# Performance work log

Measured on AMD Instinct MI355X. Metric: run time of the kernel, lower is better.

Reference implementation:

```python
import jax, jax.numpy as jnp
import numpy as np

NUM_USERS = 100000
NUM_ITEMS = 50000
N = NUM_USERS + NUM_ITEMS
EMB = 64
NNZ = 4000000
B = 4096
GAMMA = 1.0
REG_LAMBDA = 1e-4
T_END = 1.0  # Euler step size: t = [0, 1]
EPS = 1e-12


def setup_inputs() -> dict:
    key = jax.random.key(0)
    ks = jax.random.split(key, 8)
    user = jax.random.randint(ks[0], (B,), 0, NUM_USERS)
    positive = jax.random.randint(ks[1], (B,), 0, NUM_ITEMS)
    negative = jax.random.randint(ks[2], (B,), 0, NUM_ITEMS)
    adj_rows = jax.random.randint(ks[3], (NNZ,), 0, N)
    adj_cols = jax.random.randint(ks[4], (NNZ,), 0, N)
    # normalized-adjacency-like small positive values
    adj_vals = jax.random.uniform(ks[5], (NNZ,), jnp.float32) * 1e-3
    user_emb = jax.random.normal(ks[6], (NUM_USERS, EMB), jnp.float32) * 0.1
    item_emb = jax.random.normal(ks[7], (NUM_ITEMS, EMB), jnp.float32) * 0.1
    return {
        "user": user, "positive": positive, "negative": negative,
        "adj_rows": adj_rows, "adj_cols": adj_cols, "adj_vals": adj_vals,
        "user_emb": user_emb, "item_emb": item_emb,
    }


def _normalize(x):
    return x * jax.lax.rsqrt(jnp.sum(x * x, axis=-1, keepdims=True) + EPS)


def _uniform_loss(x):
    # log mean_{i<j} exp(-2 * ||xn_i - xn_j||^2), xn = L2-normalized
    xn = _normalize(x)
    sq = jnp.maximum(2.0 - 2.0 * (xn @ xn.T), 0.0)  # [B, B] pairwise squared dist
    mask = jnp.triu(jnp.ones((x.shape[0], x.shape[0]), bool), k=1)
    vals = jnp.where(mask, jnp.exp(-2.0 * sq), 0.0)
    n_pairs = x.shape[0] * (x.shape[0] - 1) / 2.0
    return jnp.log(jnp.sum(vals) / n_pairs)


def reference(user, positive, negative, adj_rows, adj_cols, adj_vals, user_emb, item_emb):
    # ego embeddings: concat user/item tables -> [N, EMB]
    x = jnp.concatenate([user_emb, item_emb], axis=0)
    # sparse spmm: ax = A @ x (COO gather + segment reduce)
    ax = jax.ops.segment_sum(adj_vals[:, None] * x[adj_cols], adj_rows, num_segments=N)
    # ODEFunc f(t, x) = A@x + e with e = x0; one Euler step z1 = x0 + t*(A@x0 + x0)
    z = x + T_END * (ax + x)
    u_all, i_all = z[:NUM_USERS], z[NUM_USERS:]
    u = u_all[user]          # [B, EMB]
    i = i_all[positive]      # [B, EMB]
    # alignment loss on normalized embeddings
    un, inn = _normalize(u), _normalize(i)
    align = jnp.mean(jnp.sum((un - inn) ** 2, axis=-1))
    # uniformity loss
    uniform = GAMMA * (_uniform_loss(u) + _uniform_loss(i)) / 2.0
    # L2 reg on ego (pre-propagation) embeddings
    ego_u = user_emb[user]
    ego_i = item_emb[positive]
    reg = REG_LAMBDA * 0.5 * (jnp.sum(ego_u ** 2) + jnp.sum(ego_i ** 2)) / B
    return jnp.stack([align, uniform, reg])
```

## Files before the change

kernel.cpp:

```cpp
#include <hip/hip_runtime.h>
#include <math.h>

#define NUSERS 100000
#define NITEMS 50000
#define NN (NUSERS + NITEMS)
#define EMB 64
#define NNZ_ 4000000
#define BB 4096
#define NSLOT (2 * BB)
#define CAP 128
#define FSTR 32
#define BMW 4688
#define EPSN 1e-12f
#define NT 32
#define NTRI 528


typedef __attribute__((ext_vector_type(8))) short short8v;
typedef __attribute__((ext_vector_type(16))) float f32x16;

__device__ inline float wave_reduce_sum(float v) {
  #pragma unroll
  for (int off = 32; off >= 1; off >>= 1) v += __shfl_xor(v, off, 64);
  return v;
}

__device__ inline unsigned short f2bf(float f) {
  unsigned u = __float_as_uint(f);
  unsigned r = u + 0x7fffu + ((u >> 16) & 1u);
  return (unsigned short)(r >> 16);
}

__global__ __launch_bounds__(256) void lg_init(int* map, int* fillp, unsigned* bitmap) {
  int t = blockIdx.x * blockDim.x + threadIdx.x;
  if (t < NN) map[t] = -1;
  if (t < NSLOT * FSTR) fillp[t] = 0;
  if (t < BMW) bitmap[t] = 0u;
}

__global__ __launch_bounds__(256) void lg_mark(const int* __restrict__ user,
                                               const int* __restrict__ positive,
                                               int* __restrict__ map,
                                               unsigned* __restrict__ bitmap) {
  int t = blockIdx.x * blockDim.x + threadIdx.x;
  if (t >= 2 * BB) return;
  int row = (t < BB) ? user[t] : (NUSERS + positive[t - BB]);
  atomicCAS(&map[row], -1, t);
  atomicOr(&bitmap[row >> 5], 1u << (row & 31));
}

__global__ __launch_bounds__(256) void lg_scan_bin(const int4* __restrict__ rows4,
                                                   const int4* __restrict__ cols4,
                                                   const float4* __restrict__ vals4,
                                                   const unsigned* __restrict__ bitmap,
                                                   const int* __restrict__ map,
                                                   int* __restrict__ fillp,
                                                   uint2* __restrict__ bins) {
  __shared__ int qr[4][256];
  __shared__ uint2 qcv[4][256];
  int t = threadIdx.x;
  int lane = t & 63, w = t >> 6;
  unsigned long long lmlt = (1ull << lane) - 1ull;
  const int NG = NNZ_ / 4;
  int g = blockIdx.x * 256 + t;
  bool valid = g < NG;
  int gg = valid ? g : 0;
  int4 r = rows4[gg];
  int4 c = cols4[gg];
  float4 v = vals4[gg];
  bool h0 = valid && ((bitmap[r.x >> 5] >> (r.x & 31)) & 1u);
  bool h1 = valid && ((bitmap[r.y >> 5] >> (r.y & 31)) & 1u);
  bool h2 = valid && ((bitmap[r.z >> 5] >> (r.z & 31)) & 1u);
  bool h3 = valid && ((bitmap[r.w >> 5] >> (r.w & 31)) & 1u);
  int qn = 0;
  {
    unsigned long long m = __ballot(h0);
    if (h0) { int p = qn + (int)__popcll(m & lmlt); qr[w][p] = r.x;
              qcv[w][p] = make_uint2((unsigned)c.x, __float_as_uint(v.x)); }
    qn += (int)__popcll(m);
  }
  {
    unsigned long long m = __ballot(h1);
    if (h1) { int p = qn + (int)__popcll(m & lmlt); qr[w][p] = r.y;
              qcv[w][p] = make_uint2((unsigned)c.y, __float_as_uint(v.y)); }
    qn += (int)__popcll(m);
  }
  {
    unsigned long long m = __ballot(h2);
    if (h2) { int p = qn + (int)__popcll(m & lmlt); qr[w][p] = r.z;
              qcv[w][p] = make_uint2((unsigned)c.z, __float_as_uint(v.z)); }
    qn += (int)__popcll(m);
  }
  {
    unsigned long long m = __ballot(h3);
    if (h3) { int p = qn + (int)__popcll(m & lmlt); qr[w][p] = r.w;
              qcv[w][p] = make_uint2((unsigned)c.w, __float_as_uint(v.w)); }
    qn += (int)__popcll(m);
  }
  for (int i = lane; i < qn; i += 64) {
    int rr = qr[w][i];
    uint2 cv = qcv[w][i];
    int s = map[rr];
    int pos = atomicAdd(&fillp[s * FSTR], 1);
    if (pos < CAP) bins[(size_t)s * CAP + pos] = cv;
  }
}

__global__ __launch_bounds__(256) void lg_accum(const int* __restrict__ fillp,
                                                const uint2* __restrict__ bins,
                                                const float* __restrict__ uemb,
                                                const float* __restrict__ iemb,
                                                float* __restrict__ acc) {
  int w = (blockIdx.x * blockDim.x + threadIdx.x) >> 6;
  int lane = threadIdx.x & 63;
  if (w >= NSLOT) return;
  int n = min(fillp[w * FSTR], CAP);
  const uint2* bs = bins + (size_t)w * CAP;
  float a = 0.0f;
  int k = 0;
  for (; k + 4 <= n; k += 4) {
    uint2 e0 = bs[k];
    uint2 e1 = bs[k + 1];
    uint2 e2 = bs[k + 2];
    uint2 e3 = bs[k + 3];
    int c0 = (int)e0.x; float v0 = __uint_as_float(e0.y);
    int c1 = (int)e1.x; float v1 = __uint_as_float(e1.y);
    int c2 = (int)e2.x; float v2 = __uint_as_float(e2.y);
    int c3 = (int)e3.x; float v3 = __uint_as_float(e3.y);
    const float* x0 = (c0 < NUSERS) ? uemb + (size_t)c0 * EMB : iemb + (size_t)(c0 - NUSERS) * EMB;
    const float* x1 = (c1 < NUSERS) ? uemb + (size_t)c1 * EMB : iemb + (size_t)(c1 - NUSERS) * EMB;
    const float* x2 = (c2 < NUSERS) ? uemb + (size_t)c2 * EMB : iemb + (size_t)(c2 - NUSERS) * EMB;
    const float* x3 = (c3 < NUSERS) ? uemb + (size_t)c3 * EMB : iemb + (size_t)(c3 - NUSERS) * EMB;
    float f0 = x0[lane], f1 = x1[lane], f2 = x2[lane], f3 = x3[lane];
    a = fmaf(v0, f0, a);
    a = fmaf(v1, f1, a);
    a = fmaf(v2, f2, a);
    a = fmaf(v3, f3, a);
  }
  for (; k < n; ++k) {
    uint2 e0 = bs[k];
    int c0 = (int)e0.x; float v0 = __uint_as_float(e0.y);
    const float* x0 = (c0 < NUSERS) ? uemb + (size_t)c0 * EMB : iemb + (size_t)(c0 - NUSERS) * EMB;
    a = fmaf(v0, x0[lane], a);
  }
  acc[(size_t)w * EMB + lane] = a;
}

__global__ __launch_bounds__(256) void lg_prep(const int* __restrict__ user,
                                               const int* __restrict__ positive,
                                               const float* __restrict__ uemb,
                                               const float* __restrict__ iemb,
                                               const int* __restrict__ map,
                                               const float* __restrict__ acc,
                                               unsigned short* __restrict__ zub,
                                               unsigned short* __restrict__ zib,
                                               float* __restrict__ part_align,
                                               float* __restrict__ part_reg) {
  int w = (blockIdx.x * blockDim.x + threadIdx.x) >> 6;
  int lane = threadIdx.x & 63;
  if (w >= BB) return;
  int ru = user[w];
  int pi = positive[w];
  float eu = uemb[(size_t)ru * EMB + lane];
  float ei = iemb[(size_t)pi * EMB + lane];
  int su = map[ru];
  int si = map[NUSERS + pi];
  float zul = 2.0f * eu + acc[(size_t)su * EMB + lane];
  float zil = 2.0f * ei + acc[(size_t)si * EMB + lane];
  float nu = wave_reduce_sum(zul * zul);
  float ni = wave_reduce_sum(zil * zil);
  float un = zul * rsqrtf(nu + EPSN);
  float inn = zil * rsqrtf(ni + EPSN);
  zub[(size_t)w * EMB + lane] = f2bf(un);
  zib[(size_t)w * EMB + lane] = f2bf(inn);
  float d = un - inn;
  float align_b = wave_reduce_sum(d * d);
  float reg_b = wave_reduce_sum(eu * eu + ei * ei);
  if (lane == 0) {
    part_align[w] = align_b;
    part_reg[w] = reg_b;
  }
}

__global__ __launch_bounds__(256) void lg_gram_mfma(const unsigned short* __restrict__ zub,
                                                    const unsigned short* __restrict__ zib,
                                                    float* __restrict__ gpart) {
  int L = blockIdx.x, m = blockIdx.y;
  int ib = 0, rem = L;
  while (rem >= NT - ib) { rem -= NT - ib; ++ib; }
  int jb = ib + rem;
  const unsigned short* z = (m == 0) ? zub : zib;
  __shared__ uint4 As4[1024];
  __shared__ uint4 Bs4[1024];
  __shared__ float wsum[4];
  int t = threadIdx.x;
  const uint4* srcA = (const uint4*)(z + (size_t)ib * 128 * EMB);
  const uint4* srcB = (const uint4*)(z + (size_t)jb * 128 * EMB);
  #pragma unroll
  for (int it = 0; it < 4; ++it) {
    int idx = it * 256 + t;
    int r = idx >> 3, s = idx & 7;
    int dst = r * 8 + (s ^ (r & 7));
    As4[dst] = srcA[idx];
    Bs4[dst] = srcB[idx];
  }
  __syncthreads();
  int l = t & 63, w = t >> 6;
  int wr = w >> 1, wc = w & 1;
  int lr = l & 31;
  int h = l >> 5;
  int ra0 = wr * 64 + lr;
  int ra1 = ra0 + 32;
  int rb0 = wc * 64 + lr;
  int rb1 = rb0 + 32;
  f32x16 a00 = {}, a01 = {}, a10 = {}, a11 = {};
  #pragma unroll
  for (int ks = 0; ks < 4; ++ks) {
    int seg = ks * 2 + h;
    short8v a0 = *(const short8v*)&As4[ra0 * 8 + (seg ^ (ra0 & 7))];
    short8v a1 = *(const short8v*)&As4[ra1 * 8 + (seg ^ (ra1 & 7))];
    short8v b0 = *(const short8v*)&Bs4[rb0 * 8 + (seg ^ (rb0 & 7))];
    short8v b1 = *(const short8v*)&Bs4[rb1 * 8 + (seg ^ (rb1 & 7))];
    a00 = __builtin_amdgcn_mfma_f32_32x32x16_bf16(a0, b0, a00, 0, 0, 0);
    a01 = __builtin_amdgcn_mfma_f32_32x32x16_bf16(a0, b1, a01, 0, 0, 0);
    a10 = __builtin_amdgcn_mfma_f32_32x32x16_bf16(a1, b0, a10, 0, 0, 0);
    a11 = __builtin_amdgcn_mfma_f32_32x32x16_bf16(a1, b1, a11, 0, 0, 0);
  }
  float s = 0.0f;
  #pragma unroll
  for (int e = 0; e < 16; ++e) {
    s += __expf(-2.0f * fmaxf(fmaf(-2.0f, a00[e], 2.0f), 0.0f));
    s += __expf(-2.0f * fmaxf(fmaf(-2.0f, a01[e], 2.0f), 0.0f));
    s += __expf(-2.0f * fmaxf(fmaf(-2.0f, a10[e], 2.0f), 0.0f));
    s += __expf(-2.0f * fmaxf(fmaf(-2.0f, a11[e], 2.0f), 0.0f));
  }
  s = wave_reduce_sum(s);
  if (l == 0) wsum[w] = s;
  __syncthreads();
  if (t == 0) {
    float tot = wsum[0] + wsum[1] + wsum[2] + wsum[3];
    float wgt = (ib == jb) ? 1.0f : 2.0f;
    gpart[m * NTRI + L] = wgt * tot;
  }
}

__global__ __launch_bounds__(256) void lg_final(const float* __restrict__ part_align,
                                                const float* __restrict__ part_reg,
                                                const float* __restrict__ gpart,
                                                float* __restrict__ out) {
  __shared__ float red[4][4];
  int t = threadIdx.x;
  float sa = 0.0f, sr = 0.0f, su = 0.0f, si = 0.0f;
  for (int k = t; k < 4096; k += 256) {
    sa += part_align[k];
    sr += part_reg[k];
  }
  for (int k = t; k < NTRI; k += 256) {
    su += gpart[k];
    si += gpart[NTRI + k];
  }
  sa = wave_reduce_sum(sa);
  sr = wave_reduce_sum(sr);
  su = wave_reduce_sum(su);
  si = wave_reduce_sum(si);
  if ((t & 63) == 0) {
    int wid = t >> 6;
    red[wid][0] = sa; red[wid][1] = sr; red[wid][2] = su; red[wid][3] = si;
  }
  __syncthreads();
  if (t == 0) {
    float a = 0, r = 0, Su = 0, Si = 0;
    #pragma unroll
    for (int wv = 0; wv < 4; ++wv) {
      a += red[wv][0]; r += red[wv][1]; Su += red[wv][2]; Si += red[wv][3];
    }
    float align = a / (float)BB;
    float reg = 1e-4f * 0.5f * r / (float)BB;
    float npairs = (float)BB * (float)(BB - 1) * 0.5f;
    float tri_u = (Su - (float)BB) * 0.5f;
    float tri_i = (Si - (float)BB) * 0.5f;
    float Lu = logf(tri_u / npairs);
    float Li = logf(tri_i / npairs);
    out[0] = align;
    out[1] = 0.5f * (Lu + Li);
    out[2] = reg;
  }
}

extern "C" void kernel_launch(void* const* d_in, const int* in_sizes, int n_in,
                              void* d_out, int out_size, void* d_ws, size_t ws_size,
                              hipStream_t stream) {
  const int* user = (const int*)d_in[0];
  const int* positive = (const int*)d_in[1];
  const int* adj_rows = (const int*)d_in[3];
  const int* adj_cols = (const int*)d_in[4];
  const float* adj_vals = (const float*)d_in[5];
  const float* uemb = (const float*)d_in[6];
  const float* iemb = (const float*)d_in[7];

  char* ws = (char*)d_ws;
  int* map = (int*)(ws);
  int* fillp = (int*)(ws + (1u << 20));
  uint2* bins = (uint2*)(ws + (2u << 20));
  float* acc = (float*)(ws + (10u << 20));
  unsigned short* zub = (unsigned short*)(ws + (12u << 20));
  unsigned short* zib = (unsigned short*)(ws + (12u << 20) + (512u << 10));
  float* part_align = (float*)(ws + (13u << 20));
  float* part_reg = (float*)(ws + (13u << 20) + (16u << 10));
  float* gpart = (float*)(ws + (13u << 20) + (32u << 10));
  unsigned* bitmap = (unsigned*)(ws + (13u << 20) + (64u << 10));
  float* out = (float*)d_out;

  const int NG = NNZ_ / 4;
  lg_init<<<dim3(1024), dim3(256), 0, stream>>>(map, fillp, bitmap);
  lg_mark<<<dim3(32), dim3(256), 0, stream>>>(user, positive, map, bitmap);
  lg_scan_bin<<<dim3((NG + 255) / 256), dim3(256), 0, stream>>>(
      (const int4*)adj_rows, (const int4*)adj_cols, (const float4*)adj_vals,
      bitmap, map, fillp, bins);
  lg_accum<<<dim3(NSLOT / 4), dim3(256), 0, stream>>>(fillp, bins, uemb, iemb, acc);
  lg_prep<<<dim3(1024), dim3(256), 0, stream>>>(user, positive, uemb, iemb, map,
                                                acc, zub, zib, part_align, part_reg);
  lg_gram_mfma<<<dim3(NTRI, 2), dim3(256), 0, stream>>>(zub, zib, gpart);
  lg_final<<<dim3(1), dim3(256), 0, stream>>>(part_align, part_reg, gpart, out);
}
```

Before: 62.41 us.

## Make scan-bin kernel persistent with grid-stride loop and prefetched next chunk

The COO scan/bin kernel now launches a fixed 1024-block grid, and each thread walks four strided chunks of the edge list. It prefetches the next int4/float4 rows, cols and vals while testing bitmap membership for the current chunk. The per-wave LDS queue grows to 512 entries and is flushed to the bins when nearly full, so fewer blocks are launched and load latency is hidden behind the bitmap checks. The cost is more shared memory per block, which may lower occupancy, plus the loop's serial dependency.

After: 64.83 us. 1.04x slower.

```diff
diff --git a/kernel.cpp b/kernel.cpp
--- a/kernel.cpp
+++ b/kernel.cpp
@@ -14,6 +14,8 @@
 #define EPSN 1e-12f
 #define NT 32
 #define NTRI 528
+#define SCAN_GRID 1024
+#define QCAP 512
 
 
 typedef __attribute__((ext_vector_type(8))) short short8v;
@@ -56,46 +58,66 @@
                                                    const int* __restrict__ map,
                                                    int* __restrict__ fillp,
                                                    uint2* __restrict__ bins) {
-  __shared__ int qr[4][256];
-  __shared__ uint2 qcv[4][256];
+  __shared__ int qr[4][QCAP];
+  __shared__ uint2 qcv[4][QCAP];
   int t = threadIdx.x;
   int lane = t & 63, w = t >> 6;
   unsigned long long lmlt = (1ull << lane) - 1ull;
   const int NG = NNZ_ / 4;
+  const int STR = SCAN_GRID * 256;
+  int qn = 0;
   int g = blockIdx.x * 256 + t;
-  bool valid = g < NG;
-  int gg = valid ? g : 0;
-  int4 r = rows4[gg];
-  int4 c = cols4[gg];
-  float4 v = vals4[gg];
-  bool h0 = valid && ((bitmap[r.x >> 5] >> (r.x & 31)) & 1u);
-  bool h1 = valid && ((bitmap[r.y >> 5] >> (r.y & 31)) & 1u);
-  bool h2 = valid && ((bitmap[r.z >> 5] >> (r.z & 31)) & 1u);
-  bool h3 = valid && ((bitmap[r.w >> 5] >> (r.w & 31)) & 1u);
-  int qn = 0;
-  {
-    unsigned long long m = __ballot(h0);
-    if (h0) { int p = qn + (int)__popcll(m & lmlt); qr[w][p] = r.x;
-              qcv[w][p] = make_uint2((unsigned)c.x, __float_as_uint(v.x)); }
-    qn += (int)__popcll(m);
-  }
-  {
-    unsigned long long m = __ballot(h1);
-    if (h1) { int p = qn + (int)__popcll(m & lmlt); qr[w][p] = r.y;
-              qcv[w][p] = make_uint2((unsigned)c.y, __float_as_uint(v.y)); }
-    qn += (int)__popcll(m);
-  }
-  {
-    unsigned long long m = __ballot(h2);
-    if (h2) { int p = qn + (int)__popcll(m & lmlt); qr[w][p] = r.z;
-              qcv[w][p] = make_uint2((unsigned)c.z, __float_as_uint(v.z)); }
-    qn += (int)__popcll(m);
-  }
-  {
-    unsigned long long m = __ballot(h3);
-    if (h3) { int p = qn + (int)__popcll(m & lmlt); qr[w][p] = r.w;
-              qcv[w][p] = make_uint2((unsigned)c.w, __float_as_uint(v.w)); }
-    qn += (int)__popcll(m);
+  bool valid = true;
+  int4 r = rows4[g];
+  int4 c = cols4[g];
+  float4 v = vals4[g];
+  #pragma unroll 1
+  for (int it = 0; it < 4; ++it) {
+    int gn = g + STR;
+    bool vok = (it < 3) & (gn < NG);
+    int gnc = vok ? gn : 0;
+    int4 rn = rows4[gnc];
+    int4 cn = cols4[gnc];
+    float4 vn = vals4[gnc];
+    bool h0 = valid && ((bitmap[r.x >> 5] >> (r.x & 31)) & 1u);
+    bool h1 = valid && ((bitmap[r.y >> 5] >> (r.y & 31)) & 1u);
+    bool h2 = valid && ((bitmap[r.z >> 5] >> (r.z & 31)) & 1u);
+    bool h3 = valid && ((bitmap[r.w >> 5] >> (r.w & 31)) & 1u);
+    if (qn > QCAP - 256) {
+      for (int i = lane; i < qn; i += 64) {
+        int rr = qr[w][i];
+        uint2 cv = qcv[w][i];
+        int s = map[rr];
+        int pos = atomicAdd(&fillp[s * FSTR], 1);
+        if (pos < CAP) bins[(size_t)s * CAP + pos] = cv;
+      }
+      qn = 0;
+    }
+    {
+      unsigned long long m = __ballot(h0);
+      if (h0) { int p = qn + (int)__popcll(m & lmlt); qr[w][p] = r.x;
+                qcv[w][p] = make_uint2((unsigned)c.x, __float_as_uint(v.x)); }
+      qn += (int)__popcll(m);
+    }
+    {
+      unsigned long long m = __ballot(h1);
+      if (h1) { int p = qn + (int)__popcll(m & lmlt); qr[w][p] = r.y;
+                qcv[w][p] = make_uint2((unsigned)c.y, __float_as_uint(v.y)); }
+      qn += (int)__popcll(m);
+    }
+    {
+      unsigned long long m = __ballot(h2);
+      if (h2) { int p = qn + (int)__popcll(m & lmlt); qr[w][p] = r.z;
+                qcv[w][p] = make_uint2((unsigned)c.z, __float_as_uint(v.z)); }
+      qn += (int)__popcll(m);
+    }
+    {
+      unsigned long long m = __ballot(h3);
+      if (h3) { int p = qn + (int)__popcll(m & lmlt); qr[w][p] = r.w;
+                qcv[w][p] = make_uint2((unsigned)c.w, __float_as_uint(v.w)); }
+      qn += (int)__popcll(m);
+    }
+    r = rn; c = cn; v = vn; valid = vok; g = gn;
   }
   for (int i = lane; i < qn; i += 64) {
     int rr = qr[w][i];
@@ -311,10 +333,9 @@
   unsigned* bitmap = (unsigned*)(ws + (13u << 20) + (64u << 10));
   float* out = (float*)d_out;
 
-  const int NG = NNZ_ / 4;
   lg_init<<<dim3(1024), dim3(256), 0, stream>>>(map, fillp, bitmap);
   lg_mark<<<dim3(32), dim3(256), 0, stream>>>(user, positive, map, bitmap);
-  lg_scan_bin<<<dim3((NG + 255) / 256), dim3(256), 0, stream>>>(
+  lg_scan_bin<<<dim3(SCAN_GRID), dim3(256), 0, stream>>>(
       (const int4*)adj_rows, (const int4*)adj_cols, (const float4*)adj_vals,
       bitmap, map, fillp, bins);
   lg_accum<<<dim3(NSLOT / 4), dim3(256), 0, stream>>>(fillp, bins, uemb, iemb, acc);
```

## Split edge scan into row-probe pass and sparse collect of hit edges

Applied to the files above, without the earlier changes.

Replaces the single scan kernel, which streamed rows, cols and vals for all 4M edges, with two kernels. A probe kernel reads only the rows array and writes a one-byte hit mask per group of four edges. A collect kernel then reads cols and vals only for edges whose row is in the batch, since hits are sparse (about 5% of rows). This removes most of the cols/vals bandwidth, at the cost of an extra launch, a mask round trip through memory, and scattered single-element loads.

Measured after the change: 69.36 us. +11.1%, slower.

```diff
diff --git a/kernel.cpp b/kernel.cpp
--- a/kernel.cpp
+++ b/kernel.cpp
@@ -14,6 +14,8 @@
 #define EPSN 1e-12f
 #define NT 32
 #define NTRI 528
+#define NG (NNZ_ / 4)
+#define NM4 (NG / 4)
 
 
 typedef __attribute__((ext_vector_type(8))) short short8v;
@@ -49,60 +51,51 @@
   atomicOr(&bitmap[row >> 5], 1u << (row & 31));
 }
 
-__global__ __launch_bounds__(256) void lg_scan_bin(const int4* __restrict__ rows4,
-                                                   const int4* __restrict__ cols4,
-                                                   const float4* __restrict__ vals4,
-                                                   const unsigned* __restrict__ bitmap,
-                                                   const int* __restrict__ map,
-                                                   int* __restrict__ fillp,
-                                                   uint2* __restrict__ bins) {
-  __shared__ int qr[4][256];
-  __shared__ uint2 qcv[4][256];
+__global__ __launch_bounds__(256) void lg_probe(const int4* __restrict__ rows4,
+                                                const unsigned* __restrict__ bitmap,
+                                                unsigned char* __restrict__ mask) {
+  int t = blockIdx.x * 256 + threadIdx.x;
+  if (t >= NG) return;
+  int4 r = rows4[t];
+  unsigned h = ((bitmap[r.x >> 5] >> (r.x & 31)) & 1u)
+             | (((bitmap[r.y >> 5] >> (r.y & 31)) & 1u) << 1)
+             | (((bitmap[r.z >> 5] >> (r.z & 31)) & 1u) << 2)
+             | (((bitmap[r.w >> 5] >> (r.w & 31)) & 1u) << 3);
+  mask[t] = (unsigned char)h;
+}
+
+__global__ __launch_bounds__(256) void lg_collect(const unsigned* __restrict__ mask4,
+                                                  const int* __restrict__ rows,
+                                                  const int* __restrict__ cols,
+                                                  const float* __restrict__ vals,
+                                                  const int* __restrict__ map,
+                                                  int* __restrict__ fillp,
+                                                  uint2* __restrict__ bins) {
+  __shared__ int qk[4][1024];
+  __shared__ int qn[4];
   int t = threadIdx.x;
   int lane = t & 63, w = t >> 6;
-  unsigned long long lmlt = (1ull << lane) - 1ull;
-  const int NG = NNZ_ / 4;
+  if (lane == 0) qn[w] = 0;
+  __syncthreads();
   int g = blockIdx.x * 256 + t;
-  bool valid = g < NG;
-  int gg = valid ? g : 0;
-  int4 r = rows4[gg];
-  int4 c = cols4[gg];
-  float4 v = vals4[gg];
-  bool h0 = valid && ((bitmap[r.x >> 5] >> (r.x & 31)) & 1u);
-  bool h1 = valid && ((bitmap[r.y >> 5] >> (r.y & 31)) & 1u);
-  bool h2 = valid && ((bitmap[r.z >> 5] >> (r.z & 31)) & 1u);
-  bool h3 = valid && ((bitmap[r.w >> 5] >> (r.w & 31)) & 1u);
-  int qn = 0;
-  {
-    unsigned long long m = __ballot(h0);
-    if (h0) { int p = qn + (int)__popcll(m & lmlt); qr[w][p] = r.x;
-              qcv[w][p] = make_uint2((unsigned)c.x, __float_as_uint(v.x)); }
-    qn += (int)__popcll(m);
-  }
-  {
-    unsigned long long m = __ballot(h1);
-    if (h1) { int p = qn + (int)__popcll(m & lmlt); qr[w][p] = r.y;
-              qcv[w][p] = make_uint2((unsigned)c.y, __float_as_uint(v.y)); }
-    qn += (int)__popcll(m);
-  }
-  {
-    unsigned long long m = __ballot(h2);
-    if (h2) { int p = qn + (int)__popcll(m & lmlt); qr[w][p] = r.z;
-              qcv[w][p] = make_uint2((unsigned)c.z, __float_as_uint(v.z)); }
-    qn += (int)__popcll(m);
-  }
-  {
-    unsigned long long m = __ballot(h3);
-    if (h3) { int p = qn + (int)__popcll(m & lmlt); qr[w][p] = r.w;
-              qcv[w][p] = make_uint2((unsigned)c.w, __float_as_uint(v.w)); }
-    qn += (int)__popcll(m);
-  }
-  for (int i = lane; i < qn; i += 64) {
-    int rr = qr[w][i];
-    uint2 cv = qcv[w][i];
-    int s = map[rr];
+  unsigned m = (g < NM4) ? mask4[g] : 0u;
+  while (m) {
+    int p = __ffs(m) - 1;
+    m &= m - 1;
+    int k = g * 16 + (p >> 3) * 4 + (p & 7);
+    int pos = atomicAdd(&qn[w], 1);
+    qk[w][pos] = k;
+  }
+  __syncthreads();
+  int n = qn[w];
+  for (int i = lane; i < n; i += 64) {
+    int k = qk[w][i];
+    int r = rows[k];
+    int c = cols[k];
+    float v = vals[k];
+    int s = map[r];
     int pos = atomicAdd(&fillp[s * FSTR], 1);
-    if (pos < CAP) bins[(size_t)s * CAP + pos] = cv;
+    if (pos < CAP) bins[(size_t)s * CAP + pos] = make_uint2((unsigned)c, __float_as_uint(v));
   }
 }
 
@@ -309,14 +302,15 @@
   float* part_reg = (float*)(ws + (13u << 20) + (16u << 10));
   float* gpart = (float*)(ws + (13u << 20) + (32u << 10));
   unsigned* bitmap = (unsigned*)(ws + (13u << 20) + (64u << 10));
+  unsigned char* hitmask = (unsigned char*)(ws + (14u << 20));
   float* out = (float*)d_out;
 
-  const int NG = NNZ_ / 4;
   lg_init<<<dim3(1024), dim3(256), 0, stream>>>(map, fillp, bitmap);
   lg_mark<<<dim3(32), dim3(256), 0, stream>>>(user, positive, map, bitmap);
-  lg_scan_bin<<<dim3((NG + 255) / 256), dim3(256), 0, stream>>>(
-      (const int4*)adj_rows, (const int4*)adj_cols, (const float4*)adj_vals,
-      bitmap, map, fillp, bins);
+  lg_probe<<<dim3((NG + 255) / 256), dim3(256), 0, stream>>>(
+      (const int4*)adj_rows, bitmap, hitmask);
+  lg_collect<<<dim3((NM4 + 255) / 256), dim3(256), 0, stream>>>(
+      (const unsigned*)hitmask, adj_rows, adj_cols, adj_vals, map, fillp, bins);
   lg_accum<<<dim3(NSLOT / 4), dim3(256), 0, stream>>>(fillp, bins, uemb, iemb, acc);
   lg_prep<<<dim3(1024), dim3(256), 0, stream>>>(user, positive, uemb, iemb, map,
                                                 acc, zub, zib, part_align, part_reg);
```
